# Optimization experiments

Hardware: AMD Instinct MI355X
Metric: run time of the kernel (lower is better)

Reference implementation:

```python
import jax, jax.numpy as jnp
import numpy as np

LN_EPS = 1e-5


def _layernorm(x, w, b):
    m = jnp.mean(x, axis=-1, keepdims=True)
    v = jnp.mean(jnp.square(x - m), axis=-1, keepdims=True)
    return (x - m) * jax.lax.rsqrt(v + LN_EPS) * w + b


def setup_inputs() -> dict:
    key = jax.random.key(0)
    k1, k2 = jax.random.split(key)
    B, S, D = 64, 512, 1024
    inputo = jax.random.normal(k1, (B, S, D), dtype=jnp.float32)
    W = jax.random.normal(k2, (2 * D, 4 * D), dtype=jnp.float32) * 0.02
    b = jnp.zeros((4 * D,), dtype=jnp.float32)
    ln_w = jnp.ones((4 * D,), dtype=jnp.float32)
    ln_b = jnp.zeros((4 * D,), dtype=jnp.float32)
    init_hx = jnp.zeros((1, D), dtype=jnp.float32)
    init_cx = jnp.zeros((1, D), dtype=jnp.float32)
    return {"inputo": inputo, "W": W, "b": b, "ln_w": ln_w, "ln_b": ln_b,
            "init_hx": init_hx, "init_cx": init_cx}


def reference(inputo, W, b, ln_w, ln_b, init_hx, init_cx):
    B, S, D = inputo.shape
    osize = init_hx.shape[1]
    hx = jnp.broadcast_to(init_hx, (B, osize))
    cx = jnp.broadcast_to(init_cx, (B, osize))

    def step(carry, x_t):
        h, c = carry
        comb = _layernorm(jnp.concatenate([x_t, h], axis=-1) @ W + b, ln_w, ln_b)
        comb = comb.reshape(B, 4, osize)
        gates = jax.nn.sigmoid(comb[:, :3])          # ig, fg, og
        hidden = jnp.tanh(comb[:, 3])
        c = gates[:, 1] * c + gates[:, 0] * hidden
        h = gates[:, 2] * jnp.tanh(c)
        return (h, c), h

    xs = jnp.swapaxes(inputo, 0, 1)                  # [S, B, D]
    _, outs = jax.lax.scan(step, (hx, cx), xs)       # [S, B, osize]
    return jnp.swapaxes(outs, 0, 1)                  # [B, S, osize]
```

## Files before the change

kernel.cpp:

```cpp
#include <hip/hip_runtime.h>
#include <hip/hip_bf16.h>


typedef __attribute__((ext_vector_type(8))) short bf16x8;
typedef __attribute__((ext_vector_type(16))) float f32x16;
typedef __attribute__((ext_vector_type(4)))  int   i32x4;
typedef __attribute__((ext_vector_type(4)))  float f32x4;

#define AT_RLX __ATOMIC_RELAXED
#define SC_AGT __HIP_MEMORY_SCOPE_AGENT


__global__ __launch_bounds__(256) void conv_w(const float* __restrict__ W,
                                              __hip_bfloat16* __restrict__ Wt) {
    size_t id = (size_t)blockIdx.x * 256 + threadIdx.x;
    int k = (int)(id >> 12);
    int n = (int)(id & 4095);
    Wt[(size_t)n * 2048 + k] = __float2bfloat16(W[id]);
}

__global__ __launch_bounds__(256) void conv_x(const float* __restrict__ X,
                                              __hip_bfloat16* __restrict__ Xt) {
    size_t id = (size_t)blockIdx.x * 256 + threadIdx.x;
    int d   = (int)(id & 1023);
    int row = (int)(id >> 10);
    int s = row >> 6;
    int b = row & 63;
    Xt[id] = __float2bfloat16(X[(((size_t)b * 512 + s) << 10) + d]);
}

__global__ __launch_bounds__(256) void init_h(const float* __restrict__ hx,
                                              __hip_bfloat16* __restrict__ h,
                                              unsigned int* __restrict__ cflag,
                                              unsigned int* __restrict__ hflag) {
    int id = blockIdx.x * 256 + threadIdx.x;
    h[id] = __float2bfloat16(hx[id & 1023]);
    if (id < 4096) cflag[id] = 0u;
    else if (id < 5120) hflag[id - 4096] = 0u;
}

__device__ __forceinline__ i32x4 ld_cp16(const void* p) {
    i32x4 r;
    asm volatile("global_load_dwordx4 %0, %1, off sc0 sc1"
                 : "=&v"(r) : "v"(p) : "memory");
    return r;
}
__device__ __forceinline__ void vm_wait0() {
    asm volatile("s_waitcnt vmcnt(0)" ::: "memory");
    __builtin_amdgcn_sched_barrier(0);
}
__device__ __forceinline__ void xchg8f(float* p, float lo, float hi) {
    union { float f[2]; unsigned long long u; } c;
    c.f[0] = lo; c.f[1] = hi;
    unsigned long long old =
        __hip_atomic_exchange((unsigned long long*)p, c.u, AT_RLX, SC_AGT);
    asm volatile("" :: "v"(old));
}
__device__ __forceinline__ void xchg8u(unsigned long long* p, unsigned long long v) {
    unsigned long long old = __hip_atomic_exchange(p, v, AT_RLX, SC_AGT);
    asm volatile("" :: "v"(old));
}

__global__ __launch_bounds__(256, 1) void lstm_fused(
    const __hip_bfloat16* __restrict__ Xt,
    const __hip_bfloat16* __restrict__ Wt,
    __hip_bfloat16* __restrict__ h,
    const float* __restrict__ bias,
    const float* __restrict__ lnw,
    const float* __restrict__ lnb,
    const float* __restrict__ cx,
    float* __restrict__ comb,
    float* __restrict__ out,
    unsigned int* __restrict__ cflag,
    unsigned int* __restrict__ hflag)
{
    const int tid  = threadIdx.x;
    const int lane = tid & 63;
    const int wv   = tid >> 6;
    const int b    = blockIdx.x;

    const int nt = b >> 1;
    const int mt = b & 1;
    const int kc = wv;
    const int cl = lane & 31;
    const int kh = (lane >> 5) * 8;
    const int n0 = nt * 32;

    __shared__ float lds_f[4096];
    __shared__ float red[8];

    const short* bp = (const short*)Wt + (size_t)(n0 + cl) * 2048 + kc * 512 + kh;
    bf16x8 breg[32];
#pragma unroll
    for (int i = 0; i < 32; ++i) breg[i] = *(const bf16x8*)(bp + i * 16);

    const short* xbase = (const short*)Xt + (size_t)(mt * 32 + cl) * 1024 + kc * 512 + kh;
    const short* hrow  = (const short*)h  + (size_t)(mt * 32 + cl) * 1024 + (kc - 2) * 512 + kh;
    const unsigned int* myhf = &hflag[(mt * 32 + cl) * 16];
    const unsigned int* mycf = &cflag[(2 * (tid & 127) + (b >> 5)) * 16];

    float cr[4];
    f32x4 bias_r[4], lnw_r[4], lnb_r[4];
    if (b < 64) {
#pragma unroll
        for (int e = 0; e < 4; ++e) cr[e] = cx[4 * tid + e];
#pragma unroll
        for (int g = 0; g < 4; ++g) {
            bias_r[g] = *(const f32x4*)&bias[1024 * g + 4 * tid];
            lnw_r[g]  = *(const f32x4*)&lnw[1024 * g + 4 * tid];
            lnb_r[g]  = *(const f32x4*)&lnb[1024 * g + 4 * tid];
        }
    }

    for (int s = 0; s < 512; ++s) {
        f32x16 accA, accB;
#pragma unroll
        for (int i = 0; i < 16; ++i) { accA[i] = 0.f; accB[i] = 0.f; }
        if (kc < 2) {
            const short* ap = xbase + (size_t)s * 65536;
#pragma unroll
            for (int i = 0; i < 16; ++i) {
                bf16x8 a0 = *(const bf16x8*)(ap + i * 16);
                bf16x8 a1 = *(const bf16x8*)(ap + (i + 16) * 16);
                accA = __builtin_amdgcn_mfma_f32_32x32x16_bf16(a0, breg[i],      accA, 0, 0, 0);
                accB = __builtin_amdgcn_mfma_f32_32x32x16_bf16(a1, breg[i + 16], accB, 0, 0, 0);
            }
        } else {
            while (__hip_atomic_load(myhf, AT_RLX, SC_AGT) < (unsigned int)s)
                __builtin_amdgcn_s_sleep(1);
            asm volatile("" ::: "memory");
            bf16x8 ha[32];
#pragma unroll
            for (int i = 0; i < 32; ++i)
                ha[i] = __builtin_bit_cast(bf16x8, ld_cp16(hrow + i * 16));
            vm_wait0();
#pragma unroll
            for (int i = 0; i < 16; ++i) {
                accA = __builtin_amdgcn_mfma_f32_32x32x16_bf16(ha[i],      breg[i],      accA, 0, 0, 0);
                accB = __builtin_amdgcn_mfma_f32_32x32x16_bf16(ha[i + 16], breg[i + 16], accB, 0, 0, 0);
            }
        }
#pragma unroll
        for (int r = 0; r < 16; ++r) {
            int rl = (r & 3) + 8 * (r >> 2) + 4 * (lane >> 5);
            lds_f[kc * 1024 + rl * 32 + cl] = accA[r] + accB[r];
        }
        __syncthreads();
        {
            float* crow = comb + (size_t)(mt * 32) * 4096 + n0;
#pragma unroll
            for (int half = 0; half < 2; ++half) {
                int e = 2 * tid + half * 512;
                float2 p0 = *(const float2*)&lds_f[e];
                float2 p1 = *(const float2*)&lds_f[1024 + e];
                float2 p2 = *(const float2*)&lds_f[2048 + e];
                float2 p3 = *(const float2*)&lds_f[3072 + e];
                xchg8f(&crow[(size_t)(e >> 5) * 4096 + (e & 31)],
                       p0.x + p1.x + p2.x + p3.x,
                       p0.y + p1.y + p2.y + p3.y);
            }
        }
        __syncthreads();
        if (tid == 0)
            __hip_atomic_store(&cflag[b * 16], (unsigned int)(s + 1), AT_RLX, SC_AGT);

        if (b < 64) {
            if (tid < 128) {
                while (__hip_atomic_load(mycf, AT_RLX, SC_AGT) < (unsigned int)(s + 1))
                    __builtin_amdgcn_s_sleep(1);
            }
            __syncthreads();
            asm volatile("" ::: "memory");
            const float* c0 = comb + (size_t)b * 4096;
            f32x4 xv[4];
#pragma unroll
            for (int g = 0; g < 4; ++g)
                xv[g] = __builtin_bit_cast(f32x4, ld_cp16(&c0[1024 * g + 4 * tid]));
            vm_wait0();
            float v[4][4];
            float s1 = 0.f, s2 = 0.f;
#pragma unroll
            for (int g = 0; g < 4; ++g)
#pragma unroll
                for (int e = 0; e < 4; ++e) {
                    float x = xv[g][e] + bias_r[g][e];
                    v[g][e] = x;
                    s1 += x;
                    s2 += x * x;
                }
            for (int off = 32; off; off >>= 1) {
                s1 += __shfl_down(s1, off);
                s2 += __shfl_down(s2, off);
            }
            if (lane == 0) { red[2 * wv] = s1; red[2 * wv + 1] = s2; }
            __syncthreads();
            float sum = red[0] + red[2] + red[4] + red[6];
            float ssq = red[1] + red[3] + red[5] + red[7];
            float mean = sum * (1.f / 4096.f);
            float var  = ssq * (1.f / 4096.f) - mean * mean;
            float rstd = rsqrtf(var + 1e-5f);
            float hn[4];
#pragma unroll
            for (int e = 0; e < 4; ++e) {
                float yi = (v[0][e] - mean) * rstd * lnw_r[0][e] + lnb_r[0][e];
                float yf = (v[1][e] - mean) * rstd * lnw_r[1][e] + lnb_r[1][e];
                float yo = (v[2][e] - mean) * rstd * lnw_r[2][e] + lnb_r[2][e];
                float yh = (v[3][e] - mean) * rstd * lnw_r[3][e] + lnb_r[3][e];
                float ig = 1.f / (1.f + __expf(-yi));
                float fg = 1.f / (1.f + __expf(-yf));
                float og = 1.f / (1.f + __expf(-yo));
                float hd = tanhf(yh);
                float cn = fg * cr[e] + ig * hd;
                cr[e] = cn;
                hn[e] = og * tanhf(cn);
            }
            unsigned long long hp = 0;
#pragma unroll
            for (int e = 0; e < 4; ++e)
                hp |= (unsigned long long)
                      __builtin_bit_cast(unsigned short, __float2bfloat16(hn[e])) << (16 * e);
            xchg8u((unsigned long long*)((unsigned short*)h + b * 1024 + 4 * tid), hp);
            __syncthreads();
            if (tid == 0)
                __hip_atomic_store(&hflag[b * 16], (unsigned int)(s + 1), AT_RLX, SC_AGT);
            f32x4 o4;
#pragma unroll
            for (int e = 0; e < 4; ++e) o4[e] = hn[e];
            *(f32x4*)(out + (size_t)b * 524288 + (size_t)s * 1024 + 4 * tid) = o4;
        }
    }
}

extern "C" void kernel_launch(void* const* d_in, const int* in_sizes, int n_in,
                              void* d_out, int out_size, void* d_ws, size_t ws_size,
                              hipStream_t stream) {
    const float* X   = (const float*)d_in[0];
    const float* W   = (const float*)d_in[1];
    const float* bv  = (const float*)d_in[2];
    const float* lnw = (const float*)d_in[3];
    const float* lnb = (const float*)d_in[4];
    const float* hx  = (const float*)d_in[5];
    const float* cx  = (const float*)d_in[6];
    float* out = (float*)d_out;

    char* base = (char*)d_ws;
    __hip_bfloat16* Wt    = (__hip_bfloat16*)(base);
    __hip_bfloat16* Xt    = (__hip_bfloat16*)(base + 16777216);
    float*          comb  = (float*)         (base + 83886080);
    __hip_bfloat16* hbuf  = (__hip_bfloat16*)(base + 84934656);
    unsigned int*   cflag = (unsigned int*)  (base + 85065728);
    unsigned int*   hflag = (unsigned int*)  (base + 85082112);

    conv_w<<<32768, 256, 0, stream>>>(W, Wt);
    conv_x<<<131072, 256, 0, stream>>>(X, Xt);
    init_h<<<256, 256, 0, stream>>>(hx, hbuf, cflag, hflag);

    lstm_fused<<<256, 256, 0, stream>>>(Xt, Wt, hbuf, bv, lnw, lnb, cx, comb, out,
                                        cflag, hflag);
}
```

Before: 5.549 ms.

## Replace flag-based cross-block sync with NaN-sentinel data polling and h ring buffer

Drops the per-step cflag/hflag counters and the barriers around them. Consumers now poll the data itself: the comb and h buffers are pre-filled with a NaN sentinel, readers reload until no sentinel is left, then reset the slot to the sentinel. h is kept in a 3-slot ring so producers and readers of adjacent steps do not overwrite each other, and the LDS reduction buffer is double-buffered so a barrier can be removed. The aim is to cut the flag-store/flag-poll round trips and extra __syncthreads on the serial step path. It relies on real results never matching the sentinel bit pattern, and the repeated polling reloads add memory traffic.

```diff
diff --git a/kernel.cpp b/kernel.cpp
--- a/kernel.cpp
+++ b/kernel.cpp
@@ -9,6 +9,10 @@
 
 #define AT_RLX __ATOMIC_RELAXED
 #define SC_AGT __HIP_MEMORY_SCOPE_AGENT
+
+struct U2 { unsigned long long a, b; };
+#define BF16SENT4 0x7FC07FC07FC07FC0ULL
+#define F32SENT2  0x7FC000007FC00000ULL
 
 
 __global__ __launch_bounds__(256) void conv_w(const float* __restrict__ W,
@@ -29,14 +33,19 @@
     Xt[id] = __float2bfloat16(X[(((size_t)b * 512 + s) << 10) + d]);
 }
 
-__global__ __launch_bounds__(256) void init_h(const float* __restrict__ hx,
-                                              __hip_bfloat16* __restrict__ h,
-                                              unsigned int* __restrict__ cflag,
-                                              unsigned int* __restrict__ hflag) {
+__global__ __launch_bounds__(256) void init_rings(const float* __restrict__ hx,
+                                                  unsigned int* __restrict__ combu,
+                                                  unsigned int* __restrict__ hru) {
     int id = blockIdx.x * 256 + threadIdx.x;
-    h[id] = __float2bfloat16(hx[id & 1023]);
-    if (id < 4096) cflag[id] = 0u;
-    else if (id < 5120) hflag[id - 4096] = 0u;
+    if (id >= 360448) return;
+    if (id < 262144) { combu[id] = 0x7FC00000u; return; }
+    int j = id - 262144;
+    if (j < 65536) { hru[j] = 0x7FC07FC0u; return; }
+    int j2 = j - 65536;
+    int d = (j2 & 511) * 2;
+    unsigned int lo = __builtin_bit_cast(unsigned short, __float2bfloat16(hx[d]));
+    unsigned int hi = __builtin_bit_cast(unsigned short, __float2bfloat16(hx[d + 1]));
+    hru[65536 + j2] = lo | (hi << 16);
 }
 
 __device__ __forceinline__ i32x4 ld_cp16(const void* p) {
@@ -64,15 +73,13 @@
 __global__ __launch_bounds__(256, 1) void lstm_fused(
     const __hip_bfloat16* __restrict__ Xt,
     const __hip_bfloat16* __restrict__ Wt,
-    __hip_bfloat16* __restrict__ h,
     const float* __restrict__ bias,
     const float* __restrict__ lnw,
     const float* __restrict__ lnb,
     const float* __restrict__ cx,
     float* __restrict__ comb,
-    float* __restrict__ out,
-    unsigned int* __restrict__ cflag,
-    unsigned int* __restrict__ hflag)
+    unsigned short* __restrict__ hring,
+    float* __restrict__ out)
 {
     const int tid  = threadIdx.x;
     const int lane = tid & 63;
@@ -86,7 +93,7 @@
     const int kh = (lane >> 5) * 8;
     const int n0 = nt * 32;
 
-    __shared__ float lds_f[4096];
+    __shared__ float lds_f[8192];
     __shared__ float red[8];
 
     const short* bp = (const short*)Wt + (size_t)(n0 + cl) * 2048 + kc * 512 + kh;
@@ -95,9 +102,7 @@
     for (int i = 0; i < 32; ++i) breg[i] = *(const bf16x8*)(bp + i * 16);
 
     const short* xbase = (const short*)Xt + (size_t)(mt * 32 + cl) * 1024 + kc * 512 + kh;
-    const short* hrow  = (const short*)h  + (size_t)(mt * 32 + cl) * 1024 + (kc - 2) * 512 + kh;
-    const unsigned int* myhf = &hflag[(mt * 32 + cl) * 16];
-    const unsigned int* mycf = &cflag[(2 * (tid & 127) + (b >> 5)) * 16];
+    const unsigned short* hrow = hring + (mt * 32 + cl) * 1024 + (kc - 2) * 512 + kh;
 
     float cr[4];
     f32x4 bias_r[4], lnw_r[4], lnb_r[4];
@@ -111,6 +116,9 @@
             lnb_r[g]  = *(const f32x4*)&lnb[1024 * g + 4 * tid];
         }
     }
+
+    int sr = 2;
+    int sw = 0;
 
     for (int s = 0; s < 512; ++s) {
         f32x16 accA, accB;
@@ -126,24 +134,37 @@
                 accB = __builtin_amdgcn_mfma_f32_32x32x16_bf16(a1, breg[i + 16], accB, 0, 0, 0);
             }
         } else {
-            while (__hip_atomic_load(myhf, AT_RLX, SC_AGT) < (unsigned int)s)
+            const unsigned short* hp = hrow + sr * 65536;
+            bf16x8 ha[32];
+            unsigned int miss = 0xFFFFFFFFu;
+            for (;;) {
+#pragma unroll
+                for (int i = 0; i < 32; ++i)
+                    if (miss & (1u << i))
+                        ha[i] = __builtin_bit_cast(bf16x8, ld_cp16(hp + i * 16));
+                vm_wait0();
+                unsigned int nm = 0;
+#pragma unroll
+                for (int i = 0; i < 32; ++i)
+                    if (miss & (1u << i)) {
+                        U2 c = __builtin_bit_cast(U2, ha[i]);
+                        if (c.a == BF16SENT4 || c.b == BF16SENT4) nm |= 1u << i;
+                    }
+                miss = nm;
+                if (!miss) break;
                 __builtin_amdgcn_s_sleep(1);
-            asm volatile("" ::: "memory");
-            bf16x8 ha[32];
-#pragma unroll
-            for (int i = 0; i < 32; ++i)
-                ha[i] = __builtin_bit_cast(bf16x8, ld_cp16(hrow + i * 16));
-            vm_wait0();
+            }
 #pragma unroll
             for (int i = 0; i < 16; ++i) {
                 accA = __builtin_amdgcn_mfma_f32_32x32x16_bf16(ha[i],      breg[i],      accA, 0, 0, 0);
                 accB = __builtin_amdgcn_mfma_f32_32x32x16_bf16(ha[i + 16], breg[i + 16], accB, 0, 0, 0);
             }
         }
+        float* lbuf = lds_f + (s & 1) * 4096;
 #pragma unroll
         for (int r = 0; r < 16; ++r) {
             int rl = (r & 3) + 8 * (r >> 2) + 4 * (lane >> 5);
-            lds_f[kc * 1024 + rl * 32 + cl] = accA[r] + accB[r];
+            lbuf[kc * 1024 + rl * 32 + cl] = accA[r] + accB[r];
         }
         __syncthreads();
         {
@@ -151,32 +172,46 @@
 #pragma unroll
             for (int half = 0; half < 2; ++half) {
                 int e = 2 * tid + half * 512;
-                float2 p0 = *(const float2*)&lds_f[e];
-                float2 p1 = *(const float2*)&lds_f[1024 + e];
-                float2 p2 = *(const float2*)&lds_f[2048 + e];
-                float2 p3 = *(const float2*)&lds_f[3072 + e];
+                float2 p0 = *(const float2*)&lbuf[e];
+                float2 p1 = *(const float2*)&lbuf[1024 + e];
+                float2 p2 = *(const float2*)&lbuf[2048 + e];
+                float2 p3 = *(const float2*)&lbuf[3072 + e];
                 xchg8f(&crow[(size_t)(e >> 5) * 4096 + (e & 31)],
                        p0.x + p1.x + p2.x + p3.x,
                        p0.y + p1.y + p2.y + p3.y);
             }
         }
-        __syncthreads();
-        if (tid == 0)
-            __hip_atomic_store(&cflag[b * 16], (unsigned int)(s + 1), AT_RLX, SC_AGT);
 
         if (b < 64) {
-            if (tid < 128) {
-                while (__hip_atomic_load(mycf, AT_RLX, SC_AGT) < (unsigned int)(s + 1))
-                    __builtin_amdgcn_s_sleep(1);
-            }
-            __syncthreads();
-            asm volatile("" ::: "memory");
             const float* c0 = comb + (size_t)b * 4096;
             f32x4 xv[4];
-#pragma unroll
-            for (int g = 0; g < 4; ++g)
-                xv[g] = __builtin_bit_cast(f32x4, ld_cp16(&c0[1024 * g + 4 * tid]));
-            vm_wait0();
+            unsigned int miss = 0xFu;
+            for (;;) {
+#pragma unroll
+                for (int g = 0; g < 4; ++g)
+                    if (miss & (1u << g))
+                        xv[g] = __builtin_bit_cast(f32x4, ld_cp16(&c0[1024 * g + 4 * tid]));
+                vm_wait0();
+                unsigned int nm = 0;
+#pragma unroll
+                for (int g = 0; g < 4; ++g)
+                    if (miss & (1u << g)) {
+                        U2 c = __builtin_bit_cast(U2, xv[g]);
+                        if (c.a == F32SENT2 || c.b == F32SENT2) nm |= 1u << g;
+                    }
+                miss = nm;
+                if (!miss) break;
+                __builtin_amdgcn_s_sleep(1);
+            }
+            __syncthreads();
+            {
+                float* crst = (float*)c0 + 16 * tid;
+#pragma unroll
+                for (int j = 0; j < 8; ++j)
+                    xchg8u((unsigned long long*)(crst + 2 * j), F32SENT2);
+                xchg8u((unsigned long long*)(hring + sr * 65536 + b * 1024 + 4 * tid),
+                       BF16SENT4);
+            }
             float v[4][4];
             float s1 = 0.f, s2 = 0.f;
 #pragma unroll
@@ -214,20 +249,19 @@
                 cr[e] = cn;
                 hn[e] = og * tanhf(cn);
             }
-            unsigned long long hp = 0;
+            unsigned long long hp8 = 0;
 #pragma unroll
             for (int e = 0; e < 4; ++e)
-                hp |= (unsigned long long)
-                      __builtin_bit_cast(unsigned short, __float2bfloat16(hn[e])) << (16 * e);
-            xchg8u((unsigned long long*)((unsigned short*)h + b * 1024 + 4 * tid), hp);
-            __syncthreads();
-            if (tid == 0)
-                __hip_atomic_store(&hflag[b * 16], (unsigned int)(s + 1), AT_RLX, SC_AGT);
+                hp8 |= (unsigned long long)
+                       __builtin_bit_cast(unsigned short, __float2bfloat16(hn[e])) << (16 * e);
+            xchg8u((unsigned long long*)(hring + sw * 65536 + b * 1024 + 4 * tid), hp8);
             f32x4 o4;
 #pragma unroll
             for (int e = 0; e < 4; ++e) o4[e] = hn[e];
             *(f32x4*)(out + (size_t)b * 524288 + (size_t)s * 1024 + 4 * tid) = o4;
         }
+        sr = (sr == 2) ? 0 : sr + 1;
+        sw = (sw == 2) ? 0 : sw + 1;
     }
 }
 
@@ -247,14 +281,11 @@
     __hip_bfloat16* Wt    = (__hip_bfloat16*)(base);
     __hip_bfloat16* Xt    = (__hip_bfloat16*)(base + 16777216);
     float*          comb  = (float*)         (base + 83886080);
-    __hip_bfloat16* hbuf  = (__hip_bfloat16*)(base + 84934656);
-    unsigned int*   cflag = (unsigned int*)  (base + 85065728);
-    unsigned int*   hflag = (unsigned int*)  (base + 85082112);
+    unsigned short* hring = (unsigned short*)(base + 84934656);
 
     conv_w<<<32768, 256, 0, stream>>>(W, Wt);
     conv_x<<<131072, 256, 0, stream>>>(X, Xt);
-    init_h<<<256, 256, 0, stream>>>(hx, hbuf, cflag, hflag);
-
-    lstm_fused<<<256, 256, 0, stream>>>(Xt, Wt, hbuf, bv, lnw, lnb, cx, comb, out,
-                                        cflag, hflag);
-}
+    init_rings<<<1408, 256, 0, stream>>>(hx, (unsigned int*)comb, (unsigned int*)hring);
+
+    lstm_fused<<<256, 256, 0, stream>>>(Xt, Wt, bv, lnw, lnb, cx, comb, hring, out);
+}
```

Result: slower. 7.535 ms (+35.8%).

## Replace per-block completion flags with epoch-tagged 64-bit combo values

Applied to the files above, without the earlier changes.

Each partial GEMM result is now stored as a 64-bit word that carries the step number in its upper half and the float in its lower half. Consumers poll the data itself until every element they need shows the current epoch. This removes the second block barrier and the separate cflag store/poll round trip. The LDS staging buffer is double-buffered by step parity so the next step's writes cannot race with readers still in the previous step. In exchange the comb traffic doubles (64-bit entries) and each consumer thread issues 16 polling atomic loads instead of one flag check plus four vector loads.

```diff
diff --git a/kernel.cpp b/kernel.cpp
--- a/kernel.cpp
+++ b/kernel.cpp
@@ -5,7 +5,6 @@
 typedef __attribute__((ext_vector_type(8))) short bf16x8;
 typedef __attribute__((ext_vector_type(16))) float f32x16;
 typedef __attribute__((ext_vector_type(4)))  int   i32x4;
-typedef __attribute__((ext_vector_type(4)))  float f32x4;
 
 #define AT_RLX __ATOMIC_RELAXED
 #define SC_AGT __HIP_MEMORY_SCOPE_AGENT
@@ -29,14 +28,14 @@
     Xt[id] = __float2bfloat16(X[(((size_t)b * 512 + s) << 10) + d]);
 }
 
-__global__ __launch_bounds__(256) void init_h(const float* __restrict__ hx,
-                                              __hip_bfloat16* __restrict__ h,
-                                              unsigned int* __restrict__ cflag,
-                                              unsigned int* __restrict__ hflag) {
+__global__ __launch_bounds__(256) void init_misc(const float* __restrict__ hx,
+                                                 __hip_bfloat16* __restrict__ h,
+                                                 unsigned long long* __restrict__ comb2,
+                                                 unsigned int* __restrict__ hflag) {
     int id = blockIdx.x * 256 + threadIdx.x;
-    h[id] = __float2bfloat16(hx[id & 1023]);
-    if (id < 4096) cflag[id] = 0u;
-    else if (id < 5120) hflag[id - 4096] = 0u;
+    comb2[id] = 0ULL;
+    if (id < 65536) h[id] = __float2bfloat16(hx[id & 1023]);
+    if (id < 1024)  hflag[id] = 0u;
 }
 
 __device__ __forceinline__ i32x4 ld_cp16(const void* p) {
@@ -48,13 +47,6 @@
 __device__ __forceinline__ void vm_wait0() {
     asm volatile("s_waitcnt vmcnt(0)" ::: "memory");
     __builtin_amdgcn_sched_barrier(0);
-}
-__device__ __forceinline__ void xchg8f(float* p, float lo, float hi) {
-    union { float f[2]; unsigned long long u; } c;
-    c.f[0] = lo; c.f[1] = hi;
-    unsigned long long old =
-        __hip_atomic_exchange((unsigned long long*)p, c.u, AT_RLX, SC_AGT);
-    asm volatile("" :: "v"(old));
 }
 __device__ __forceinline__ void xchg8u(unsigned long long* p, unsigned long long v) {
     unsigned long long old = __hip_atomic_exchange(p, v, AT_RLX, SC_AGT);
@@ -69,9 +61,8 @@
     const float* __restrict__ lnw,
     const float* __restrict__ lnb,
     const float* __restrict__ cx,
-    float* __restrict__ comb,
+    unsigned long long* __restrict__ comb2,
     float* __restrict__ out,
-    unsigned int* __restrict__ cflag,
     unsigned int* __restrict__ hflag)
 {
     const int tid  = threadIdx.x;
@@ -86,7 +77,7 @@
     const int kh = (lane >> 5) * 8;
     const int n0 = nt * 32;
 
-    __shared__ float lds_f[4096];
+    __shared__ float lds_f[8192];
     __shared__ float red[8];
 
     const short* bp = (const short*)Wt + (size_t)(n0 + cl) * 2048 + kc * 512 + kh;
@@ -97,19 +88,20 @@
     const short* xbase = (const short*)Xt + (size_t)(mt * 32 + cl) * 1024 + kc * 512 + kh;
     const short* hrow  = (const short*)h  + (size_t)(mt * 32 + cl) * 1024 + (kc - 2) * 512 + kh;
     const unsigned int* myhf = &hflag[(mt * 32 + cl) * 16];
-    const unsigned int* mycf = &cflag[(2 * (tid & 127) + (b >> 5)) * 16];
 
     float cr[4];
-    f32x4 bias_r[4], lnw_r[4], lnb_r[4];
+    float bias_r[4][4], lnw_r[4][4], lnb_r[4][4];
     if (b < 64) {
 #pragma unroll
         for (int e = 0; e < 4; ++e) cr[e] = cx[4 * tid + e];
 #pragma unroll
-        for (int g = 0; g < 4; ++g) {
-            bias_r[g] = *(const f32x4*)&bias[1024 * g + 4 * tid];
-            lnw_r[g]  = *(const f32x4*)&lnw[1024 * g + 4 * tid];
-            lnb_r[g]  = *(const f32x4*)&lnb[1024 * g + 4 * tid];
-        }
+        for (int g = 0; g < 4; ++g)
+#pragma unroll
+            for (int e = 0; e < 4; ++e) {
+                bias_r[g][e] = bias[1024 * g + 4 * tid + e];
+                lnw_r[g][e]  = lnw[1024 * g + 4 * tid + e];
+                lnb_r[g][e]  = lnb[1024 * g + 4 * tid + e];
+            }
     }
 
     for (int s = 0; s < 512; ++s) {
@@ -140,50 +132,64 @@
                 accB = __builtin_amdgcn_mfma_f32_32x32x16_bf16(ha[i + 16], breg[i + 16], accB, 0, 0, 0);
             }
         }
+        float* lbuf = lds_f + (s & 1) * 4096;
 #pragma unroll
         for (int r = 0; r < 16; ++r) {
             int rl = (r & 3) + 8 * (r >> 2) + 4 * (lane >> 5);
-            lds_f[kc * 1024 + rl * 32 + cl] = accA[r] + accB[r];
+            lbuf[kc * 1024 + rl * 32 + cl] = accA[r] + accB[r];
         }
         __syncthreads();
         {
-            float* crow = comb + (size_t)(mt * 32) * 4096 + n0;
+            unsigned long long ep64 = ((unsigned long long)(unsigned)(s + 1)) << 32;
 #pragma unroll
             for (int half = 0; half < 2; ++half) {
                 int e = 2 * tid + half * 512;
-                float2 p0 = *(const float2*)&lds_f[e];
-                float2 p1 = *(const float2*)&lds_f[1024 + e];
-                float2 p2 = *(const float2*)&lds_f[2048 + e];
-                float2 p3 = *(const float2*)&lds_f[3072 + e];
-                xchg8f(&crow[(size_t)(e >> 5) * 4096 + (e & 31)],
-                       p0.x + p1.x + p2.x + p3.x,
-                       p0.y + p1.y + p2.y + p3.y);
-            }
-        }
-        __syncthreads();
-        if (tid == 0)
-            __hip_atomic_store(&cflag[b * 16], (unsigned int)(s + 1), AT_RLX, SC_AGT);
+                float2 p0 = *(const float2*)&lbuf[e];
+                float2 p1 = *(const float2*)&lbuf[1024 + e];
+                float2 p2 = *(const float2*)&lbuf[2048 + e];
+                float2 p3 = *(const float2*)&lbuf[3072 + e];
+                float v0 = p0.x + p1.x + p2.x + p3.x;
+                float v1 = p0.y + p1.y + p2.y + p3.y;
+                size_t g = (size_t)(mt * 32 + (e >> 5)) * 4096 + n0 + (e & 31);
+                __hip_atomic_store(&comb2[g],
+                    ep64 | __builtin_bit_cast(unsigned int, v0), AT_RLX, SC_AGT);
+                __hip_atomic_store(&comb2[g + 1],
+                    ep64 | __builtin_bit_cast(unsigned int, v1), AT_RLX, SC_AGT);
+            }
+        }
 
         if (b < 64) {
-            if (tid < 128) {
-                while (__hip_atomic_load(mycf, AT_RLX, SC_AGT) < (unsigned int)(s + 1))
-                    __builtin_amdgcn_s_sleep(1);
-            }
-            __syncthreads();
-            asm volatile("" ::: "memory");
-            const float* c0 = comb + (size_t)b * 4096;
-            f32x4 xv[4];
-#pragma unroll
-            for (int g = 0; g < 4; ++g)
-                xv[g] = __builtin_bit_cast(f32x4, ld_cp16(&c0[1024 * g + 4 * tid]));
-            vm_wait0();
+            const unsigned long long* c2 = comb2 + (size_t)b * 4096;
+            unsigned long long q[16];
+            unsigned int miss = 0xFFFFu;
+            const unsigned int tgt = (unsigned int)(s + 1);
+            for (;;) {
+#pragma unroll
+                for (int g = 0; g < 4; ++g)
+#pragma unroll
+                    for (int e = 0; e < 4; ++e) {
+                        int k = 4 * g + e;
+                        if (miss & (1u << k))
+                            q[k] = __hip_atomic_load(&c2[1024 * g + 4 * tid + e],
+                                                     AT_RLX, SC_AGT);
+                    }
+                unsigned int nm = 0;
+#pragma unroll
+                for (int k = 0; k < 16; ++k)
+                    if ((miss & (1u << k)) && (unsigned int)(q[k] >> 32) < tgt)
+                        nm |= 1u << k;
+                miss = nm;
+                if (!miss) break;
+                __builtin_amdgcn_s_sleep(1);
+            }
             float v[4][4];
             float s1 = 0.f, s2 = 0.f;
 #pragma unroll
             for (int g = 0; g < 4; ++g)
 #pragma unroll
                 for (int e = 0; e < 4; ++e) {
-                    float x = xv[g][e] + bias_r[g][e];
+                    float x = __builtin_bit_cast(float, (unsigned int)q[4 * g + e])
+                            + bias_r[g][e];
                     v[g][e] = x;
                     s1 += x;
                     s2 += x * x;
@@ -223,10 +229,11 @@
             __syncthreads();
             if (tid == 0)
                 __hip_atomic_store(&hflag[b * 16], (unsigned int)(s + 1), AT_RLX, SC_AGT);
-            f32x4 o4;
+            float o4[4];
 #pragma unroll
             for (int e = 0; e < 4; ++e) o4[e] = hn[e];
-            *(f32x4*)(out + (size_t)b * 524288 + (size_t)s * 1024 + 4 * tid) = o4;
+            *(float4*)(out + (size_t)b * 524288 + (size_t)s * 1024 + 4 * tid) =
+                *(float4*)o4;
         }
     }
 }
@@ -244,17 +251,16 @@
     float* out = (float*)d_out;
 
     char* base = (char*)d_ws;
-    __hip_bfloat16* Wt    = (__hip_bfloat16*)(base);
-    __hip_bfloat16* Xt    = (__hip_bfloat16*)(base + 16777216);
-    float*          comb  = (float*)         (base + 83886080);
-    __hip_bfloat16* hbuf  = (__hip_bfloat16*)(base + 84934656);
-    unsigned int*   cflag = (unsigned int*)  (base + 85065728);
-    unsigned int*   hflag = (unsigned int*)  (base + 85082112);
+    __hip_bfloat16*     Wt    = (__hip_bfloat16*)    (base);
+    __hip_bfloat16*     Xt    = (__hip_bfloat16*)    (base + 16777216);
+    unsigned long long* comb2 = (unsigned long long*)(base + 83886080);
+    __hip_bfloat16*     hbuf  = (__hip_bfloat16*)    (base + 85983232);
+    unsigned int*       hflag = (unsigned int*)      (base + 86114304);
 
     conv_w<<<32768, 256, 0, stream>>>(W, Wt);
     conv_x<<<131072, 256, 0, stream>>>(X, Xt);
-    init_h<<<256, 256, 0, stream>>>(hx, hbuf, cflag, hflag);
-
-    lstm_fused<<<256, 256, 0, stream>>>(Xt, Wt, hbuf, bv, lnw, lnb, cx, comb, out,
-                                        cflag, hflag);
-}
+    init_misc<<<1024, 256, 0, stream>>>(hx, hbuf, comb2, hflag);
+
+    lstm_fused<<<256, 256, 0, stream>>>(Xt, Wt, hbuf, bv, lnw, lnb, cx, comb2, out,
+                                        hflag);
+}
```

Measured after the change: 5.568 ms. No clear change (+0.4%).
